# Optimization experiments

Measured on AMD Instinct MI355X. Metric: run time of the kernel, lower is better.

The kernel has to match this reference:

```python
import jax, jax.numpy as jnp
import numpy as np

NUM_FIELDS = 32
FIELD_DIM = 50000
EMB_DIM = 64
ATT_DIM = 32
BATCH = 8192
VOCAB = NUM_FIELDS * FIELD_DIM


def setup_inputs() -> dict:
    key = jax.random.key(0)
    ks = jax.random.split(key, 8)
    x = jax.random.randint(ks[0], (BATCH, NUM_FIELDS), 0, FIELD_DIM, dtype=jnp.int64 if jax.config.read('jax_enable_x64') else jnp.int32)
    emb_table = jax.random.normal(ks[1], (VOCAB, EMB_DIM), dtype=jnp.float32) * 0.01
    lin_table = jax.random.normal(ks[2], (VOCAB, 1), dtype=jnp.float32) * 0.01
    lin_bias = jnp.zeros((1,), dtype=jnp.float32)
    W1 = jax.random.normal(ks[3], (EMB_DIM, ATT_DIM), dtype=jnp.float32) * (1.0 / np.sqrt(EMB_DIM))
    b1 = jnp.zeros((ATT_DIM,), dtype=jnp.float32)
    w2 = jax.random.normal(ks[4], (ATT_DIM,), dtype=jnp.float32) * (1.0 / np.sqrt(ATT_DIM))
    proj_w = jax.random.normal(ks[5], (EMB_DIM,), dtype=jnp.float32) * (1.0 / np.sqrt(EMB_DIM))
    return {"x": x, "emb_table": emb_table, "lin_table": lin_table, "lin_bias": lin_bias,
            "W1": W1, "b1": b1, "w2": w2, "proj_w": proj_w}


def reference(x, emb_table, lin_table, lin_bias, W1, b1, w2, proj_w):
    # per-field offsets into the concatenated vocab
    offsets = jnp.arange(NUM_FIELDS, dtype=x.dtype) * FIELD_DIM
    idx = x + offsets[None, :]                       # [B, F]

    # first-order linear term: sum over fields + bias -> [B, 1]
    first = jnp.sum(lin_table[idx], axis=1) + lin_bias

    # embeddings [B, F, D]
    emb = emb_table[idx]

    # all field pairs (i < j)
    row, col = jnp.triu_indices(NUM_FIELDS, k=1)     # each [P], P = F*(F-1)/2
    p = emb[:, row, :] * emb[:, col, :]              # [B, P, D]

    # attention MLP: Linear -> ReLU -> Linear(no bias) -> Softmax over pairs
    h = jax.nn.relu(jnp.einsum('bpd,da->bpa', p, W1) + b1)   # [B, P, A]
    scores = jnp.einsum('bpa,a->bp', h, w2)                  # [B, P]
    attn = jax.nn.softmax(scores, axis=1)[..., None]         # [B, P, 1]
    # dropout is identity in eval mode

    pooled = jnp.sum(p * attn, axis=1)               # [B, D]
    second = jnp.einsum('bd,d->b', pooled, proj_w)[:, None]  # [B, 1]

    y = first + second                               # [B, 1]
    return jax.nn.sigmoid(jnp.squeeze(y, axis=1))    # [B]
```

## Files before the change

### kernel.cpp

```cpp
#include <hip/hip_runtime.h>
#include <hip/hip_bf16.h>

#define NF 32
#define ED 64
#define AD 32
#define FD 50000
#define ROWP 68
#define SCP 36

typedef __attribute__((ext_vector_type(8))) short bf16x8;
typedef __attribute__((ext_vector_type(4))) float f32x4;

__device__ __forceinline__ short f2bf(float f) {
    union { float f; unsigned u; } v; v.f = f;
    unsigned r = v.u + 0x7fffu + ((v.u >> 16) & 1u);
    return (short)(r >> 16);
}

__global__ __launch_bounds__(256) void afm_kernel(
    const int* __restrict__ x,
    const float* __restrict__ emb_table,
    const float* __restrict__ lin_table,
    const float* __restrict__ lin_bias,
    const float* __restrict__ W1,
    const float* __restrict__ b1,
    const float* __restrict__ w2,
    const float* __restrict__ proj_w,
    float* __restrict__ out)
{
    __shared__ float s_emb[NF * ROWP];
    __shared__ float s_sc[NF * SCP];
    __shared__ float s_lin[NF];
    __shared__ float s_red[8];

    const int t    = threadIdx.x;
    const int lane = t & 63;
    const int wave = t >> 6;
    const int l15  = lane & 15;
    const int quad = lane >> 4;
    const int s    = blockIdx.x;

    {
        const int row = t >> 3, part = t & 7;
        const int gidx = x[s * NF + row] + row * FD;
        const float* rp = emb_table + (size_t)gidx * ED + part * 8;
        float4 a = *(const float4*)rp;
        float4 b = *(const float4*)(rp + 4);
        *(float4*)(s_emb + row * ROWP + part * 8)     = a;
        *(float4*)(s_emb + row * ROWP + part * 8 + 4) = b;
        if (part == 0) s_lin[row] = lin_table[gidx];
    }
    for (int idx = t; idx < NF * SCP; idx += 256) s_sc[idx] = -1e30f;

    bf16x8 w1f[2][2];
    #pragma unroll
    for (int kk = 0; kk < 2; ++kk)
        #pragma unroll
        for (int nt = 0; nt < 2; ++nt) {
            bf16x8 f;
            #pragma unroll
            for (int jj = 0; jj < 8; ++jj)
                f[jj] = f2bf(W1[(kk * 32 + quad * 8 + jj) * AD + nt * 16 + l15]);
            w1f[kk][nt] = f;
        }
    const float b1v0 = b1[l15], b1v1 = b1[16 + l15];
    const float w2v0 = w2[l15], w2v1 = w2[16 + l15];

    __syncthreads();

    float ef[2][2][8];
    #pragma unroll
    for (int jb = 0; jb < 2; ++jb)
        #pragma unroll
        for (int kk = 0; kk < 2; ++kk) {
            const float* p = s_emb + (16 * jb + l15) * ROWP + kk * 32 + quad * 8;
            float4 a = *(const float4*)p;
            float4 b = *(const float4*)(p + 4);
            ef[jb][kk][0] = a.x; ef[jb][kk][1] = a.y; ef[jb][kk][2] = a.z; ef[jb][kk][3] = a.w;
            ef[jb][kk][4] = b.x; ef[jb][kk][5] = b.y; ef[jb][kk][6] = b.z; ef[jb][kk][7] = b.w;
        }

    for (int i = wave; i < 32; i += 4) {
        float ei[2][8];
        #pragma unroll
        for (int kk = 0; kk < 2; ++kk) {
            const float* p = s_emb + i * ROWP + kk * 32 + quad * 8;
            float4 a = *(const float4*)p;
            float4 b = *(const float4*)(p + 4);
            ei[kk][0]=a.x; ei[kk][1]=a.y; ei[kk][2]=a.z; ei[kk][3]=a.w;
            ei[kk][4]=b.x; ei[kk][5]=b.y; ei[kk][6]=b.z; ei[kk][7]=b.w;
        }
        #pragma unroll
        for (int jb = 0; jb < 2; ++jb) {
            if (jb * 16 + 15 <= i) continue;
            f32x4 acc0 = {0.f,0.f,0.f,0.f}, acc1 = {0.f,0.f,0.f,0.f};
            #pragma unroll
            for (int kk = 0; kk < 2; ++kk) {
                bf16x8 af;
                #pragma unroll
                for (int jj = 0; jj < 8; ++jj)
                    af[jj] = f2bf(ei[kk][jj] * ef[jb][kk][jj]);
                acc0 = __builtin_amdgcn_mfma_f32_16x16x32_bf16(af, w1f[kk][0], acc0, 0, 0, 0);
                acc1 = __builtin_amdgcn_mfma_f32_16x16x32_bf16(af, w1f[kk][1], acc1, 0, 0, 0);
            }
            float4 scv;
            #pragma unroll
            for (int r = 0; r < 4; ++r) {
                float v = fmaxf(acc0[r] + b1v0, 0.f) * w2v0
                        + fmaxf(acc1[r] + b1v1, 0.f) * w2v1;
                v += __shfl_xor(v, 1);
                v += __shfl_xor(v, 2);
                v += __shfl_xor(v, 4);
                v += __shfl_xor(v, 8);
                const int j = jb * 16 + quad * 4 + r;
                (&scv.x)[r] = (j > i) ? v : -1e30f;
            }
            if (l15 == 0)
                *(float4*)(s_sc + i * SCP + jb * 16 + quad * 4) = scv;
        }
    }
    __syncthreads();

    float mx = -1e30f;
    for (int idx = t; idx < NF * SCP; idx += 256) mx = fmaxf(mx, s_sc[idx]);
    #pragma unroll
    for (int d = 1; d < 64; d <<= 1) mx = fmaxf(mx, __shfl_xor(mx, d));
    if (lane == 0) s_red[wave] = mx;
    __syncthreads();
    mx = fmaxf(fmaxf(s_red[0], s_red[1]), fmaxf(s_red[2], s_red[3]));
    float lsum = 0.f;
    for (int idx = t; idx < NF * SCP; idx += 256) {
        float e = __expf(s_sc[idx] - mx);
        s_sc[idx] = e;
        lsum += e;
    }
    #pragma unroll
    for (int d = 1; d < 64; d <<= 1) lsum += __shfl_xor(lsum, d);
    if (lane == 0) s_red[4 + wave] = lsum;
    __syncthreads();

    const int dcol = wave * 16 + l15;
    bf16x8 bE;
    #pragma unroll
    for (int jj = 0; jj < 8; ++jj)
        bE[jj] = f2bf(s_emb[(quad * 8 + jj) * ROWP + dcol]);
    float sec = 0.f;
    #pragma unroll
    for (int mt = 0; mt < 2; ++mt) {
        const float* ap = s_sc + (16 * mt + l15) * SCP + quad * 8;
        float4 a0 = *(const float4*)ap;
        float4 a1 = *(const float4*)(ap + 4);
        bf16x8 aA;
        aA[0]=f2bf(a0.x); aA[1]=f2bf(a0.y); aA[2]=f2bf(a0.z); aA[3]=f2bf(a0.w);
        aA[4]=f2bf(a1.x); aA[5]=f2bf(a1.y); aA[6]=f2bf(a1.z); aA[7]=f2bf(a1.w);
        f32x4 u = {0.f,0.f,0.f,0.f};
        u = __builtin_amdgcn_mfma_f32_16x16x32_bf16(aA, bE, u, 0, 0, 0);
        #pragma unroll
        for (int r = 0; r < 4; ++r)
            sec += u[r] * s_emb[(16 * mt + quad * 4 + r) * ROWP + dcol];
    }
    sec *= proj_w[dcol];
    #pragma unroll
    for (int d = 1; d < 64; d <<= 1) sec += __shfl_xor(sec, d);
    if (lane == 0) s_red[wave] = sec;
    __syncthreads();

    if (t == 0) {
        float S = s_red[4] + s_red[5] + s_red[6] + s_red[7];
        float second = (s_red[0] + s_red[1] + s_red[2] + s_red[3]) / S;
        float first = lin_bias[0];
        #pragma unroll
        for (int f = 0; f < NF; ++f) first += s_lin[f];
        float y = first + second;
        out[s] = 1.f / (1.f + __expf(-y));
    }
}

extern "C" void kernel_launch(void* const* d_in, const int* in_sizes, int n_in,
                              void* d_out, int out_size, void* d_ws, size_t ws_size,
                              hipStream_t stream) {
    const int*   x         = (const int*)d_in[0];
    const float* emb_table = (const float*)d_in[1];
    const float* lin_table = (const float*)d_in[2];
    const float* lin_bias  = (const float*)d_in[3];
    const float* W1        = (const float*)d_in[4];
    const float* b1        = (const float*)d_in[5];
    const float* w2        = (const float*)d_in[6];
    const float* proj_w    = (const float*)d_in[7];
    float* out = (float*)d_out;

    afm_kernel<<<out_size, 256, 0, stream>>>(x, emb_table, lin_table, lin_bias,
                                             W1, b1, w2, proj_w, out);
}
```

Before: 562.7 us.

## Drop softmax max pass, fuse exp into score loop, precompute bf16 W1 fragments

Computes exp of each attention score directly inside the MFMA score loop and accumulates the partial sums there. This removes the separate max-reduction pass, its extra block barrier, and the second sweep over shared memory. The lane-replicated sum is corrected by a factor of 1/16. A small prep kernel converts W1 to bf16 MFMA fragments once, so every block loads them instead of doing strided gathers and conversions, and bf16 packing uses the paired conversion intrinsic. The cost is the loss of max-subtraction for numerical stability, which could overflow if scores are large, plus one extra kernel launch.

```diff
diff --git a/kernel.cpp b/kernel.cpp
--- a/kernel.cpp
+++ b/kernel.cpp
@@ -17,12 +17,39 @@
     return (short)(r >> 16);
 }
 
+__device__ __forceinline__ bf16x8 pack8(const float* p) {
+    bf16x8 r;
+#pragma unroll
+    for (int i = 0; i < 4; ++i) {
+        __hip_bfloat162 h = __float22bfloat162_rn(make_float2(p[2*i], p[2*i+1]));
+        short2 s2 = *reinterpret_cast<short2*>(&h);
+        r[2*i] = s2.x; r[2*i+1] = s2.y;
+    }
+    return r;
+}
+
+__global__ __launch_bounds__(64) void prep_w1(const float* __restrict__ W1,
+                                              short* __restrict__ w1ws) {
+    const int lane = threadIdx.x;
+    const int l15 = lane & 15, quad = lane >> 4;
+#pragma unroll
+    for (int kk = 0; kk < 2; ++kk)
+#pragma unroll
+        for (int nt = 0; nt < 2; ++nt) {
+            bf16x8 f;
+#pragma unroll
+            for (int jj = 0; jj < 8; ++jj)
+                f[jj] = f2bf(W1[(kk * 32 + quad * 8 + jj) * AD + nt * 16 + l15]);
+            *(bf16x8*)(w1ws + ((kk * 2 + nt) * 64 + lane) * 8) = f;
+        }
+}
+
 __global__ __launch_bounds__(256) void afm_kernel(
     const int* __restrict__ x,
     const float* __restrict__ emb_table,
     const float* __restrict__ lin_table,
     const float* __restrict__ lin_bias,
-    const float* __restrict__ W1,
+    const short* __restrict__ w1ws,
     const float* __restrict__ b1,
     const float* __restrict__ w2,
     const float* __restrict__ proj_w,
@@ -40,6 +67,15 @@
     const int quad = lane >> 4;
     const int s    = blockIdx.x;
 
+    const bf16x8* wp = (const bf16x8*)w1ws;
+    bf16x8 w1f[2][2];
+    w1f[0][0] = wp[0 * 64 + lane];
+    w1f[0][1] = wp[1 * 64 + lane];
+    w1f[1][0] = wp[2 * 64 + lane];
+    w1f[1][1] = wp[3 * 64 + lane];
+    const float b1v0 = b1[l15], b1v1 = b1[16 + l15];
+    const float w2v0 = w2[l15], w2v1 = w2[16 + l15];
+
     {
         const int row = t >> 3, part = t & 7;
         const int gidx = x[s * NF + row] + row * FD;
@@ -50,61 +86,43 @@
         *(float4*)(s_emb + row * ROWP + part * 8 + 4) = b;
         if (part == 0) s_lin[row] = lin_table[gidx];
     }
-    for (int idx = t; idx < NF * SCP; idx += 256) s_sc[idx] = -1e30f;
-
-    bf16x8 w1f[2][2];
-    #pragma unroll
-    for (int kk = 0; kk < 2; ++kk)
-        #pragma unroll
-        for (int nt = 0; nt < 2; ++nt) {
-            bf16x8 f;
-            #pragma unroll
-            for (int jj = 0; jj < 8; ++jj)
-                f[jj] = f2bf(W1[(kk * 32 + quad * 8 + jj) * AD + nt * 16 + l15]);
-            w1f[kk][nt] = f;
-        }
-    const float b1v0 = b1[l15], b1v1 = b1[16 + l15];
-    const float w2v0 = w2[l15], w2v1 = w2[16 + l15];
-
+    for (int idx = t; idx < NF * SCP; idx += 256) s_sc[idx] = 0.f;
     __syncthreads();
 
     float ef[2][2][8];
-    #pragma unroll
+#pragma unroll
     for (int jb = 0; jb < 2; ++jb)
-        #pragma unroll
+#pragma unroll
         for (int kk = 0; kk < 2; ++kk) {
             const float* p = s_emb + (16 * jb + l15) * ROWP + kk * 32 + quad * 8;
-            float4 a = *(const float4*)p;
-            float4 b = *(const float4*)(p + 4);
-            ef[jb][kk][0] = a.x; ef[jb][kk][1] = a.y; ef[jb][kk][2] = a.z; ef[jb][kk][3] = a.w;
-            ef[jb][kk][4] = b.x; ef[jb][kk][5] = b.y; ef[jb][kk][6] = b.z; ef[jb][kk][7] = b.w;
-        }
-
-    for (int i = wave; i < 32; i += 4) {
+            *(float4*)&ef[jb][kk][0] = *(const float4*)p;
+            *(float4*)&ef[jb][kk][4] = *(const float4*)(p + 4);
+        }
+
+    float lsum = 0.f;
+    for (int i = wave; i < NF; i += 4) {
         float ei[2][8];
-        #pragma unroll
+#pragma unroll
         for (int kk = 0; kk < 2; ++kk) {
             const float* p = s_emb + i * ROWP + kk * 32 + quad * 8;
-            float4 a = *(const float4*)p;
-            float4 b = *(const float4*)(p + 4);
-            ei[kk][0]=a.x; ei[kk][1]=a.y; ei[kk][2]=a.z; ei[kk][3]=a.w;
-            ei[kk][4]=b.x; ei[kk][5]=b.y; ei[kk][6]=b.z; ei[kk][7]=b.w;
-        }
-        #pragma unroll
+            *(float4*)&ei[kk][0] = *(const float4*)p;
+            *(float4*)&ei[kk][4] = *(const float4*)(p + 4);
+        }
+#pragma unroll
         for (int jb = 0; jb < 2; ++jb) {
             if (jb * 16 + 15 <= i) continue;
             f32x4 acc0 = {0.f,0.f,0.f,0.f}, acc1 = {0.f,0.f,0.f,0.f};
-            #pragma unroll
+#pragma unroll
             for (int kk = 0; kk < 2; ++kk) {
-                bf16x8 af;
-                #pragma unroll
-                for (int jj = 0; jj < 8; ++jj)
-                    af[jj] = f2bf(ei[kk][jj] * ef[jb][kk][jj]);
+                float pr[8];
+#pragma unroll
+                for (int z = 0; z < 8; ++z) pr[z] = ei[kk][z] * ef[jb][kk][z];
+                bf16x8 af = pack8(pr);
                 acc0 = __builtin_amdgcn_mfma_f32_16x16x32_bf16(af, w1f[kk][0], acc0, 0, 0, 0);
                 acc1 = __builtin_amdgcn_mfma_f32_16x16x32_bf16(af, w1f[kk][1], acc1, 0, 0, 0);
             }
-            float4 scv;
-            #pragma unroll
+            float scv[4];
+#pragma unroll
             for (int r = 0; r < 4; ++r) {
                 float v = fmaxf(acc0[r] + b1v0, 0.f) * w2v0
                         + fmaxf(acc1[r] + b1v1, 0.f) * w2v1;
@@ -113,63 +131,50 @@
                 v += __shfl_xor(v, 4);
                 v += __shfl_xor(v, 8);
                 const int j = jb * 16 + quad * 4 + r;
-                (&scv.x)[r] = (j > i) ? v : -1e30f;
+                float e = (j > i) ? __expf(v) : 0.f;
+                lsum += e;
+                scv[r] = e;
             }
             if (l15 == 0)
-                *(float4*)(s_sc + i * SCP + jb * 16 + quad * 4) = scv;
-        }
-    }
-    __syncthreads();
-
-    float mx = -1e30f;
-    for (int idx = t; idx < NF * SCP; idx += 256) mx = fmaxf(mx, s_sc[idx]);
-    #pragma unroll
-    for (int d = 1; d < 64; d <<= 1) mx = fmaxf(mx, __shfl_xor(mx, d));
-    if (lane == 0) s_red[wave] = mx;
-    __syncthreads();
-    mx = fmaxf(fmaxf(s_red[0], s_red[1]), fmaxf(s_red[2], s_red[3]));
-    float lsum = 0.f;
-    for (int idx = t; idx < NF * SCP; idx += 256) {
-        float e = __expf(s_sc[idx] - mx);
-        s_sc[idx] = e;
-        lsum += e;
-    }
-    #pragma unroll
+                *(float4*)(s_sc + i * SCP + jb * 16 + quad * 4) = *(float4*)scv;
+        }
+    }
+#pragma unroll
     for (int d = 1; d < 64; d <<= 1) lsum += __shfl_xor(lsum, d);
     if (lane == 0) s_red[4 + wave] = lsum;
     __syncthreads();
 
     const int dcol = wave * 16 + l15;
-    bf16x8 bE;
-    #pragma unroll
+    float bEv[8];
+#pragma unroll
     for (int jj = 0; jj < 8; ++jj)
-        bE[jj] = f2bf(s_emb[(quad * 8 + jj) * ROWP + dcol]);
+        bEv[jj] = s_emb[(quad * 8 + jj) * ROWP + dcol];
+    bf16x8 bE = pack8(bEv);
     float sec = 0.f;
-    #pragma unroll
+#pragma unroll
     for (int mt = 0; mt < 2; ++mt) {
         const float* ap = s_sc + (16 * mt + l15) * SCP + quad * 8;
-        float4 a0 = *(const float4*)ap;
-        float4 a1 = *(const float4*)(ap + 4);
-        bf16x8 aA;
-        aA[0]=f2bf(a0.x); aA[1]=f2bf(a0.y); aA[2]=f2bf(a0.z); aA[3]=f2bf(a0.w);
-        aA[4]=f2bf(a1.x); aA[5]=f2bf(a1.y); aA[6]=f2bf(a1.z); aA[7]=f2bf(a1.w);
+        float av[8];
+        *(float4*)&av[0] = *(const float4*)ap;
+        *(float4*)&av[4] = *(const float4*)(ap + 4);
+        bf16x8 aA = pack8(av);
         f32x4 u = {0.f,0.f,0.f,0.f};
         u = __builtin_amdgcn_mfma_f32_16x16x32_bf16(aA, bE, u, 0, 0, 0);
-        #pragma unroll
+#pragma unroll
         for (int r = 0; r < 4; ++r)
             sec += u[r] * s_emb[(16 * mt + quad * 4 + r) * ROWP + dcol];
     }
     sec *= proj_w[dcol];
-    #pragma unroll
+#pragma unroll
     for (int d = 1; d < 64; d <<= 1) sec += __shfl_xor(sec, d);
     if (lane == 0) s_red[wave] = sec;
     __syncthreads();
 
     if (t == 0) {
-        float S = s_red[4] + s_red[5] + s_red[6] + s_red[7];
+        float S = (s_red[4] + s_red[5] + s_red[6] + s_red[7]) * (1.f / 16.f);
         float second = (s_red[0] + s_red[1] + s_red[2] + s_red[3]) / S;
         float first = lin_bias[0];
-        #pragma unroll
+#pragma unroll
         for (int f = 0; f < NF; ++f) first += s_lin[f];
         float y = first + second;
         out[s] = 1.f / (1.f + __expf(-y));
@@ -188,7 +193,9 @@
     const float* w2        = (const float*)d_in[6];
     const float* proj_w    = (const float*)d_in[7];
     float* out = (float*)d_out;
-
+    short* w1ws = (short*)d_ws;
+
+    prep_w1<<<1, 64, 0, stream>>>(W1, w1ws);
     afm_kernel<<<out_size, 256, 0, stream>>>(x, emb_table, lin_table, lin_bias,
-                                             W1, b1, w2, proj_w, out);
-}
+                                             w1ws, b1, w2, proj_w, out);
+}
```

After: 557.6 us. About the same (-0.9%).
